# Kernel tuning notes

Hardware: AMD Instinct MI355X
Metric: run time of the kernel (lower is better)

## Reference

```python
import jax, jax.numpy as jnp
import numpy as np

H = 16          # num heads
HD = 64         # head dim
TEMPERATURE = 1.0
LN_EPS = 1e-5

def setup_inputs() -> dict:
    key = jax.random.key(0)
    ks = jax.random.split(key, 5)
    B, S, D = 2, 2048, 1024
    s = 1.0 / np.sqrt(D)
    return {
        "x": jax.random.normal(ks[0], (B, S, D), jnp.float32),
        "Wq": jax.random.normal(ks[1], (D, D), jnp.float32) * s,
        "bq": jnp.zeros((D,), jnp.float32),
        "Wk": jax.random.normal(ks[2], (D, D), jnp.float32) * s,
        "bk": jnp.zeros((D,), jnp.float32),
        "Wv": jax.random.normal(ks[3], (D, D), jnp.float32) * s,
        "bv": jnp.zeros((D,), jnp.float32),
        "Wo": jax.random.normal(ks[4], (D, D), jnp.float32) * s,
        "bo": jnp.zeros((D,), jnp.float32),
        "ln_gamma": jnp.ones((D,), jnp.float32),
        "ln_beta": jnp.zeros((D,), jnp.float32),
    }

def reference(x, Wq, bq, Wk, bk, Wv, bv, Wo, bo, ln_gamma, ln_beta):
    B, S, D = x.shape
    # LayerNorm (pre-attention)
    mu = jnp.mean(x, axis=-1, keepdims=True)
    var = jnp.mean(jnp.square(x - mu), axis=-1, keepdims=True)
    xn = (x - mu) * jax.lax.rsqrt(var + LN_EPS) * ln_gamma + ln_beta
    # Fused QKV projections (equivalent to H per-head Linears concatenated)
    q = (xn @ Wq + bq).reshape(B, S, H, HD)
    k = (xn @ Wk + bk).reshape(B, S, H, HD)
    v = (xn @ Wv + bv).reshape(B, S, H, HD)
    scale = np.sqrt(HD) * TEMPERATURE
    scores = jnp.einsum("bqhd,bkhd->bhqk", q, k) / scale
    attn = jax.nn.softmax(scores, axis=-1)  # dropout p=0 -> identity
    ctx = jnp.einsum("bhqk,bkhd->bqhd", attn, v).reshape(B, S, D)
    out = ctx @ Wo + bo
    return x + out
```

## Files before the change

### kernel.cpp

```cpp
#include <hip/hip_runtime.h>
#include <hip/hip_bf16.h>

#define Bc   2
#define Sc   2048
#define Dc   1024
#define Hc   16
#define HDc  64
#define MR   (Bc * Sc)
#define TBK  32

typedef __attribute__((ext_vector_type(8))) short bf16x8;
typedef __attribute__((ext_vector_type(4))) float f32x4;

__device__ __forceinline__ unsigned short f2bf(float f) {
    __hip_bfloat16 h = __float2bfloat16(f);
    return *reinterpret_cast<unsigned short*>(&h);
}

__device__ __forceinline__ void gll16(const unsigned short* g, unsigned short* l) {
    __builtin_amdgcn_global_load_lds(
        (__attribute__((address_space(1))) const unsigned int*)g,
        (__attribute__((address_space(3))) unsigned int*)l,
        16, 0, 0);
}

__global__ __launch_bounds__(256) void ln_kernel(const float* __restrict__ x,
                                                 const float* __restrict__ gamma,
                                                 const float* __restrict__ beta,
                                                 unsigned short* __restrict__ xn) {
    int row = blockIdx.x;
    int t = threadIdx.x;
    const float4* xr = (const float4*)(x + (size_t)row * Dc);
    float4 v = xr[t];
    float s  = v.x + v.y + v.z + v.w;
    float ss = v.x * v.x + v.y * v.y + v.z * v.z + v.w * v.w;
    #pragma unroll
    for (int off = 32; off; off >>= 1) {
        s  += __shfl_xor(s, off, 64);
        ss += __shfl_xor(ss, off, 64);
    }
    __shared__ float red[8];
    int w = t >> 6, lane = t & 63;
    if (lane == 0) { red[w * 2] = s; red[w * 2 + 1] = ss; }
    __syncthreads();
    s  = red[0] + red[2] + red[4] + red[6];
    ss = red[1] + red[3] + red[5] + red[7];
    float mean = s * (1.0f / Dc);
    float var  = ss * (1.0f / Dc) - mean * mean;
    float rstd = rsqrtf(var + 1e-5f);
    const float4* g4 = (const float4*)gamma;
    const float4* b4 = (const float4*)beta;
    float4 g = g4[t], bb = b4[t];
    ushort4 o;
    o.x = f2bf((v.x - mean) * rstd * g.x + bb.x);
    o.y = f2bf((v.y - mean) * rstd * g.y + bb.y);
    o.z = f2bf((v.z - mean) * rstd * g.z + bb.z);
    o.w = f2bf((v.w - mean) * rstd * g.w + bb.w);
    *(ushort4*)(xn + (size_t)row * Dc + t * 4) = o;
}

__global__ __launch_bounds__(256) void wcast_kernel(
        const float* __restrict__ W0, const float* __restrict__ W1,
        const float* __restrict__ W2, const float* __restrict__ W3,
        unsigned short* __restrict__ T0, unsigned short* __restrict__ T1,
        unsigned short* __restrict__ T2, unsigned short* __restrict__ T3) {
    int z = blockIdx.z;
    const float* W = (z == 0) ? W0 : (z == 1) ? W1 : (z == 2) ? W2 : W3;
    unsigned short* T = (z == 0) ? T0 : (z == 1) ? T1 : (z == 2) ? T2 : T3;
    __shared__ float tile[64][65];
    int kb = blockIdx.y * 64, nb = blockIdx.x * 64;
    int t = threadIdx.x;
    int r0 = t >> 4, c4 = (t & 15) * 4;
    #pragma unroll
    for (int rr = 0; rr < 4; rr++) {
        int row = rr * 16 + r0;
        float4 v = *(const float4*)(W + (size_t)(kb + row) * Dc + nb + c4);
        tile[row][c4 + 0] = v.x; tile[row][c4 + 1] = v.y;
        tile[row][c4 + 2] = v.z; tile[row][c4 + 3] = v.w;
    }
    __syncthreads();
    #pragma unroll
    for (int rr = 0; rr < 4; rr++) {
        int nrow = rr * 16 + r0;
        ushort4 o;
        o.x = f2bf(tile[c4 + 0][nrow]); o.y = f2bf(tile[c4 + 1][nrow]);
        o.z = f2bf(tile[c4 + 2][nrow]); o.w = f2bf(tile[c4 + 3][nrow]);
        *(ushort4*)(T + (size_t)(nb + nrow) * Dc + kb + c4) = o;
    }
}

__device__ __forceinline__ void gemm_core(const unsigned short* __restrict__ A,
                                          const unsigned short* __restrict__ Wt,
                                          unsigned short* As, unsigned short* Bs,
                                          int m0, int n0, f32x4 acc[4][4]) {
    int t = threadIdx.x;
    int w = t >> 6, lane = t & 63;
    int l16 = lane & 15, quad = lane >> 4;
    int wm = (w >> 1) * 64, wn = (w & 1) * 64;

    int srow = lane >> 2;
    int scol = (lane & 3) * 8;
    const unsigned short* Ag = A  + (size_t)(m0 + w * 16 + srow) * Dc + scol;
    const unsigned short* Bg = Wt + (size_t)(n0 + w * 16 + srow) * Dc + scol;
    unsigned short* Asw = As + (w * 16) * TBK;
    unsigned short* Bsw = Bs + (w * 16) * TBK;

    for (int k0 = 0; k0 < Dc; k0 += TBK) {
        gll16(Ag + k0, Asw);
        gll16(Ag + k0 + (size_t)64 * Dc, Asw + 64 * TBK);
        gll16(Bg + k0, Bsw);
        gll16(Bg + k0 + (size_t)64 * Dc, Bsw + 64 * TBK);
        __syncthreads();
        bf16x8 af[4], bfr[4];
        #pragma unroll
        for (int i = 0; i < 4; i++) {
            af[i]  = *(const bf16x8*)(As + (wm + i * 16 + l16) * TBK + quad * 8);
            bfr[i] = *(const bf16x8*)(Bs + (wn + i * 16 + l16) * TBK + quad * 8);
        }
        #pragma unroll
        for (int i = 0; i < 4; i++)
            #pragma unroll
            for (int j = 0; j < 4; j++)
                acc[i][j] = __builtin_amdgcn_mfma_f32_16x16x32_bf16(af[i], bfr[j], acc[i][j], 0, 0, 0);
        __syncthreads();
    }
}

__global__ __launch_bounds__(256) void gemm_qkv_kernel(
        const unsigned short* __restrict__ A,
        const unsigned short* __restrict__ Wqt, const unsigned short* __restrict__ Wkt,
        const unsigned short* __restrict__ Wvt,
        const float* __restrict__ bq, const float* __restrict__ bk,
        const float* __restrict__ bv,
        unsigned short* __restrict__ Qb, unsigned short* __restrict__ Kb,
        unsigned short* __restrict__ Vtb) {
    __shared__ unsigned short As[128 * TBK];
    __shared__ unsigned short Bs[128 * TBK];
    int z = blockIdx.z;
    const unsigned short* Wt = (z == 0) ? Wqt : (z == 1) ? Wkt : Wvt;
    const float* bias = (z == 0) ? bq : (z == 1) ? bk : bv;
    unsigned short* Out = (z == 0) ? Qb : (z == 1) ? Kb : Vtb;
    float outscale = (z == 0) ? 0.125f : 1.0f;

    int n0 = blockIdx.x * 128, m0 = blockIdx.y * 128;
    f32x4 acc[4][4];
    #pragma unroll
    for (int i = 0; i < 4; i++)
        #pragma unroll
        for (int j = 0; j < 4; j++) acc[i][j] = (f32x4){0.f, 0.f, 0.f, 0.f};

    gemm_core(A, Wt, As, Bs, m0, n0, acc);

    int t = threadIdx.x;
    int w = t >> 6, lane = t & 63;
    int l16 = lane & 15, quad = lane >> 4;
    int wm = (w >> 1) * 64, wn = (w & 1) * 64;
    int b = m0 >> 11;
    #pragma unroll
    for (int j = 0; j < 4; j++) {
        int col = n0 + wn + j * 16 + l16;
        float bb = bias[col];
        int h = col >> 6, d = col & 63;
        #pragma unroll
        for (int i = 0; i < 4; i++) {
            #pragma unroll
            for (int r = 0; r < 4; r++) {
                int row = m0 + wm + i * 16 + quad * 4 + r;
                int s = row & (Sc - 1);
                unsigned short v = f2bf((acc[i][j][r] + bb) * outscale);
                if (z != 2)
                    Out[(((size_t)(b * Hc + h)) * Sc + s) * HDc + d] = v;
                else
                    Out[(((size_t)(b * Hc + h)) * HDc + d) * Sc + s] = v;
            }
        }
    }
}

__global__ __launch_bounds__(256) void gemm_o_kernel(
        const unsigned short* __restrict__ A,
        const unsigned short* __restrict__ Wot,
        const float* __restrict__ bo, const float* __restrict__ resid,
        float* __restrict__ Out) {
    __shared__ unsigned short As[128 * TBK];
    __shared__ unsigned short Bs[128 * TBK];
    int n0 = blockIdx.x * 128, m0 = blockIdx.y * 128;
    f32x4 acc[4][4];
    #pragma unroll
    for (int i = 0; i < 4; i++)
        #pragma unroll
        for (int j = 0; j < 4; j++) acc[i][j] = (f32x4){0.f, 0.f, 0.f, 0.f};

    gemm_core(A, Wot, As, Bs, m0, n0, acc);

    int t = threadIdx.x;
    int w = t >> 6, lane = t & 63;
    int l16 = lane & 15, quad = lane >> 4;
    int wm = (w >> 1) * 64, wn = (w & 1) * 64;
    #pragma unroll
    for (int j = 0; j < 4; j++) {
        int col = n0 + wn + j * 16 + l16;
        float bb = bo[col];
        #pragma unroll
        for (int i = 0; i < 4; i++) {
            #pragma unroll
            for (int r = 0; r < 4; r++) {
                int row = m0 + wm + i * 16 + quad * 4 + r;
                size_t off = (size_t)row * Dc + col;
                Out[off] = acc[i][j][r] + bb + resid[off];
            }
        }
    }
}

#define BQa 64
#define BKa 64
#define LDP 72

__global__ __launch_bounds__(256, 4) void attn_mfma_kernel(
        const unsigned short* __restrict__ Q,
        const unsigned short* __restrict__ K,
        const unsigned short* __restrict__ Vt,
        unsigned short* __restrict__ O) {
    __shared__ unsigned short Ks[BKa * LDP];
    __shared__ unsigned short Vs[HDc * LDP];
    __shared__ unsigned short Ps[4 * 16 * LDP];

    int t = threadIdx.x;
    int w = t >> 6, lane = t & 63;
    int quad = lane >> 4, l16 = lane & 15;
    int q0 = blockIdx.x * BQa;
    int bh = blockIdx.y;
    size_t qkbase = (size_t)bh * Sc * HDc;
    size_t vbase  = (size_t)bh * HDc * Sc;

    const unsigned short* qrow = Q + qkbase + (size_t)(q0 + w * 16 + l16) * HDc + quad * 8;
    bf16x8 qf0 = *(const bf16x8*)(qrow);
    bf16x8 qf1 = *(const bf16x8*)(qrow + 32);

    f32x4 Oacc[4];
    #pragma unroll
    for (int n = 0; n < 4; n++) Oacc[n] = (f32x4){0.f, 0.f, 0.f, 0.f};
    float lacc = 0.f;

    int srow = t >> 2, sseg = t & 3;
    const unsigned short* Kg = K + qkbase;
    const unsigned short* Vg = Vt + vbase;
    unsigned short* pw = Ps + w * 16 * LDP;

    for (int kt = 0; kt < Sc / BKa; kt++) {
        int k0 = kt * BKa;
        const unsigned short* kgp = Kg + (size_t)(k0 + srow) * HDc + sseg * 16;
        const unsigned short* vgp = Vg + (size_t)srow * Sc + k0 + sseg * 16;
        bf16x8 kv0 = *(const bf16x8*)(kgp);
        bf16x8 kv1 = *(const bf16x8*)(kgp + 8);
        bf16x8 vv0 = *(const bf16x8*)(vgp);
        bf16x8 vv1 = *(const bf16x8*)(vgp + 8);
        __syncthreads();
        *(bf16x8*)(Ks + srow * LDP + sseg * 16)     = kv0;
        *(bf16x8*)(Ks + srow * LDP + sseg * 16 + 8) = kv1;
        *(bf16x8*)(Vs + srow * LDP + sseg * 16)     = vv0;
        *(bf16x8*)(Vs + srow * LDP + sseg * 16 + 8) = vv1;
        __syncthreads();

        f32x4 st[4];
        #pragma unroll
        for (int m = 0; m < 4; m++) {
            const unsigned short* kb = Ks + (m * 16 + l16) * LDP + quad * 8;
            bf16x8 kf0 = *(const bf16x8*)(kb);
            bf16x8 kf1 = *(const bf16x8*)(kb + 32);
            f32x4 s = (f32x4){0.f, 0.f, 0.f, 0.f};
            s = __builtin_amdgcn_mfma_f32_16x16x32_bf16(kf0, qf0, s, 0, 0, 0);
            s = __builtin_amdgcn_mfma_f32_16x16x32_bf16(kf1, qf1, s, 0, 0, 0);
            st[m] = s;
        }

        #pragma unroll
        for (int m = 0; m < 4; m++) {
            float p0 = __expf(st[m][0]);
            float p1 = __expf(st[m][1]);
            float p2 = __expf(st[m][2]);
            float p3 = __expf(st[m][3]);
            lacc += (p0 + p1) + (p2 + p3);
            ushort4 pk;
            pk.x = f2bf(p0); pk.y = f2bf(p1); pk.z = f2bf(p2); pk.w = f2bf(p3);
            *(ushort4*)(pw + l16 * LDP + m * 16 + quad * 4) = pk;
        }

        #pragma unroll
        for (int kk = 0; kk < 2; kk++) {
            bf16x8 pf = *(const bf16x8*)(pw + l16 * LDP + kk * 32 + quad * 8);
            #pragma unroll
            for (int n = 0; n < 4; n++) {
                bf16x8 vf = *(const bf16x8*)(Vs + (n * 16 + l16) * LDP + kk * 32 + quad * 8);
                Oacc[n] = __builtin_amdgcn_mfma_f32_16x16x32_bf16(pf, vf, Oacc[n], 0, 0, 0);
            }
        }
    }

    lacc += __shfl_xor(lacc, 16, 64);
    lacc += __shfl_xor(lacc, 32, 64);
    int b = bh >> 4, h = bh & 15;
    #pragma unroll
    for (int i = 0; i < 4; i++) {
        float li = __shfl(lacc, quad * 4 + i, 64);
        float rl = 1.0f / li;
        int q = q0 + w * 16 + quad * 4 + i;
        #pragma unroll
        for (int n = 0; n < 4; n++) {
            O[((size_t)(b * Sc + q)) * Dc + h * HDc + n * 16 + l16] = f2bf(Oacc[n][i] * rl);
        }
    }
}

extern "C" void kernel_launch(void* const* d_in, const int* in_sizes, int n_in,
                              void* d_out, int out_size, void* d_ws, size_t ws_size,
                              hipStream_t stream) {
    const float* x     = (const float*)d_in[0];
    const float* Wq    = (const float*)d_in[1];
    const float* bq    = (const float*)d_in[2];
    const float* Wk    = (const float*)d_in[3];
    const float* bk    = (const float*)d_in[4];
    const float* Wv    = (const float*)d_in[5];
    const float* bv    = (const float*)d_in[6];
    const float* Wo    = (const float*)d_in[7];
    const float* bo    = (const float*)d_in[8];
    const float* gamma = (const float*)d_in[9];
    const float* beta  = (const float*)d_in[10];
    float* out = (float*)d_out;

    unsigned short* us = (unsigned short*)d_ws;
    const size_t NE = (size_t)MR * Dc;
    const size_t WE = (size_t)Dc * Dc;
    unsigned short* xn  = us;
    unsigned short* Qb  = us + NE;
    unsigned short* Kb  = us + 2 * NE;
    unsigned short* Vtb = us + 3 * NE;
    unsigned short* ctx = us + 4 * NE;
    unsigned short* Wqt = us + 5 * NE;
    unsigned short* Wkt = Wqt + WE;
    unsigned short* Wvt = Wkt + WE;
    unsigned short* Wot = Wvt + WE;

    dim3 tgrid(16, 16, 4);
    wcast_kernel<<<tgrid, 256, 0, stream>>>(Wq, Wk, Wv, Wo, Wqt, Wkt, Wvt, Wot);

    ln_kernel<<<MR, 256, 0, stream>>>(x, gamma, beta, xn);

    dim3 qkvgrid(Dc / 128, MR / 128, 3);
    gemm_qkv_kernel<<<qkvgrid, 256, 0, stream>>>(xn, Wqt, Wkt, Wvt, bq, bk, bv,
                                                 Qb, Kb, Vtb);

    dim3 agrid(Sc / BQa, Bc * Hc);
    attn_mfma_kernel<<<agrid, 256, 0, stream>>>(Qb, Kb, Vtb, ctx);

    dim3 ogrid(Dc / 128, MR / 128);
    gemm_o_kernel<<<ogrid, 256, 0, stream>>>(ctx, Wot, bo, x, out);
}
```

Before: 222.5 us.

## Split attention key range across waves with direct global K/V loads and reduction

Restructures the attention kernel so each of the four waves owns all 64 queries but a different 32-key slice of each 128-key step. K and V fragments are read straight from global memory instead of being staged in shared memory, which removes the per-tile __syncthreads barriers. Partial outputs and row sums are then reduced across waves through shared memory at the end. The log2(e) factor is folded into the Q scale so the kernel can call exp2 directly. In exchange it uses more registers (16 accumulators per wave, occupancy hint lowered to 3), relies on cache for K/V reuse, and adds an epilogue reduction.

```diff
diff --git a/kernel.cpp b/kernel.cpp
--- a/kernel.cpp
+++ b/kernel.cpp
@@ -8,6 +8,7 @@
 #define HDc  64
 #define MR   (Bc * Sc)
 #define TBK  32
+#define LOG2E 1.44269504088896f
 
 typedef __attribute__((ext_vector_type(8))) short bf16x8;
 typedef __attribute__((ext_vector_type(4))) float f32x4;
@@ -140,7 +141,7 @@
     const unsigned short* Wt = (z == 0) ? Wqt : (z == 1) ? Wkt : Wvt;
     const float* bias = (z == 0) ? bq : (z == 1) ? bk : bv;
     unsigned short* Out = (z == 0) ? Qb : (z == 1) ? Kb : Vtb;
-    float outscale = (z == 0) ? 0.125f : 1.0f;
+    float outscale = (z == 0) ? (0.125f * LOG2E) : 1.0f;
 
     int n0 = blockIdx.x * 128, m0 = blockIdx.y * 128;
     f32x4 acc[4][4];
@@ -213,104 +214,136 @@
     }
 }
 
-#define BQa 64
-#define BKa 64
-#define LDP 72
-
-__global__ __launch_bounds__(256, 4) void attn_mfma_kernel(
+#define PSLD 40
+
+__global__ __launch_bounds__(256, 3) void attn_mfma_kernel(
         const unsigned short* __restrict__ Q,
         const unsigned short* __restrict__ K,
         const unsigned short* __restrict__ Vt,
         unsigned short* __restrict__ O) {
-    __shared__ unsigned short Ks[BKa * LDP];
-    __shared__ unsigned short Vs[HDc * LDP];
-    __shared__ unsigned short Ps[4 * 16 * LDP];
+    __shared__ f32x4 smem[2144];
+    unsigned short* Ps = (unsigned short*)smem;
+    float* Osc  = (float*)smem;
+    float* lred = ((float*)smem) + 2 * 64 * 65;
 
     int t = threadIdx.x;
     int w = t >> 6, lane = t & 63;
     int quad = lane >> 4, l16 = lane & 15;
-    int q0 = blockIdx.x * BQa;
+    int q0 = blockIdx.x * 64;
     int bh = blockIdx.y;
-    size_t qkbase = (size_t)bh * Sc * HDc;
-    size_t vbase  = (size_t)bh * HDc * Sc;
-
-    const unsigned short* qrow = Q + qkbase + (size_t)(q0 + w * 16 + l16) * HDc + quad * 8;
-    bf16x8 qf0 = *(const bf16x8*)(qrow);
-    bf16x8 qf1 = *(const bf16x8*)(qrow + 32);
-
-    f32x4 Oacc[4];
-    #pragma unroll
-    for (int n = 0; n < 4; n++) Oacc[n] = (f32x4){0.f, 0.f, 0.f, 0.f};
-    float lacc = 0.f;
-
-    int srow = t >> 2, sseg = t & 3;
-    const unsigned short* Kg = K + qkbase;
-    const unsigned short* Vg = Vt + vbase;
-    unsigned short* pw = Ps + w * 16 * LDP;
-
-    for (int kt = 0; kt < Sc / BKa; kt++) {
-        int k0 = kt * BKa;
-        const unsigned short* kgp = Kg + (size_t)(k0 + srow) * HDc + sseg * 16;
-        const unsigned short* vgp = Vg + (size_t)srow * Sc + k0 + sseg * 16;
-        bf16x8 kv0 = *(const bf16x8*)(kgp);
-        bf16x8 kv1 = *(const bf16x8*)(kgp + 8);
-        bf16x8 vv0 = *(const bf16x8*)(vgp);
-        bf16x8 vv1 = *(const bf16x8*)(vgp + 8);
-        __syncthreads();
-        *(bf16x8*)(Ks + srow * LDP + sseg * 16)     = kv0;
-        *(bf16x8*)(Ks + srow * LDP + sseg * 16 + 8) = kv1;
-        *(bf16x8*)(Vs + srow * LDP + sseg * 16)     = vv0;
-        *(bf16x8*)(Vs + srow * LDP + sseg * 16 + 8) = vv1;
-        __syncthreads();
-
-        f32x4 st[4];
-        #pragma unroll
-        for (int m = 0; m < 4; m++) {
-            const unsigned short* kb = Ks + (m * 16 + l16) * LDP + quad * 8;
-            bf16x8 kf0 = *(const bf16x8*)(kb);
-            bf16x8 kf1 = *(const bf16x8*)(kb + 32);
-            f32x4 s = (f32x4){0.f, 0.f, 0.f, 0.f};
-            s = __builtin_amdgcn_mfma_f32_16x16x32_bf16(kf0, qf0, s, 0, 0, 0);
-            s = __builtin_amdgcn_mfma_f32_16x16x32_bf16(kf1, qf1, s, 0, 0, 0);
-            st[m] = s;
-        }
-
-        #pragma unroll
-        for (int m = 0; m < 4; m++) {
-            float p0 = __expf(st[m][0]);
-            float p1 = __expf(st[m][1]);
-            float p2 = __expf(st[m][2]);
-            float p3 = __expf(st[m][3]);
-            lacc += (p0 + p1) + (p2 + p3);
-            ushort4 pk;
-            pk.x = f2bf(p0); pk.y = f2bf(p1); pk.z = f2bf(p2); pk.w = f2bf(p3);
-            *(ushort4*)(pw + l16 * LDP + m * 16 + quad * 4) = pk;
-        }
-
-        #pragma unroll
-        for (int kk = 0; kk < 2; kk++) {
-            bf16x8 pf = *(const bf16x8*)(pw + l16 * LDP + kk * 32 + quad * 8);
-            #pragma unroll
-            for (int n = 0; n < 4; n++) {
-                bf16x8 vf = *(const bf16x8*)(Vs + (n * 16 + l16) * LDP + kk * 32 + quad * 8);
-                Oacc[n] = __builtin_amdgcn_mfma_f32_16x16x32_bf16(pf, vf, Oacc[n], 0, 0, 0);
+    const unsigned short* Qh = Q  + (size_t)bh * Sc * HDc;
+    const unsigned short* Kh = K  + (size_t)bh * Sc * HDc;
+    const unsigned short* Vh = Vt + (size_t)bh * HDc * Sc;
+
+    bf16x8 qf[4][2];
+    #pragma unroll
+    for (int j = 0; j < 4; j++) {
+        const unsigned short* qr = Qh + (size_t)(q0 + j * 16 + l16) * HDc + quad * 8;
+        qf[j][0] = *(const bf16x8*)(qr);
+        qf[j][1] = *(const bf16x8*)(qr + 32);
+    }
+
+    f32x4 Oacc[4][4];
+    #pragma unroll
+    for (int i = 0; i < 4; i++)
+        #pragma unroll
+        for (int n = 0; n < 4; n++) Oacc[i][n] = (f32x4){0.f, 0.f, 0.f, 0.f};
+    float lacc[4] = {0.f, 0.f, 0.f, 0.f};
+
+    unsigned short* Psw = Ps + w * 64 * PSLD;
+
+    for (int kt = 0; kt < Sc / 128; kt++) {
+        int k0 = kt * 128 + w * 32;
+
+        #pragma unroll
+        for (int m = 0; m < 2; m++) {
+            const unsigned short* ka = Kh + (size_t)(k0 + m * 16 + l16) * HDc + quad * 8;
+            bf16x8 kf0 = *(const bf16x8*)(ka);
+            bf16x8 kf1 = *(const bf16x8*)(ka + 32);
+            #pragma unroll
+            for (int j = 0; j < 4; j++) {
+                f32x4 s = (f32x4){0.f, 0.f, 0.f, 0.f};
+                s = __builtin_amdgcn_mfma_f32_16x16x32_bf16(kf0, qf[j][0], s, 0, 0, 0);
+                s = __builtin_amdgcn_mfma_f32_16x16x32_bf16(kf1, qf[j][1], s, 0, 0, 0);
+                float p0 = __builtin_amdgcn_exp2f(s[0]);
+                float p1 = __builtin_amdgcn_exp2f(s[1]);
+                float p2 = __builtin_amdgcn_exp2f(s[2]);
+                float p3 = __builtin_amdgcn_exp2f(s[3]);
+                lacc[j] += (p0 + p1) + (p2 + p3);
+                ushort4 pk;
+                pk.x = f2bf(p0); pk.y = f2bf(p1); pk.z = f2bf(p2); pk.w = f2bf(p3);
+                *(ushort4*)(Psw + (j * 16 + l16) * PSLD + m * 16 + quad * 4) = pk;
             }
         }
-    }
-
-    lacc += __shfl_xor(lacc, 16, 64);
-    lacc += __shfl_xor(lacc, 32, 64);
+
+        bf16x8 pf[4], vf[4];
+        #pragma unroll
+        for (int i = 0; i < 4; i++)
+            pf[i] = *(const bf16x8*)(Psw + (i * 16 + l16) * PSLD + quad * 8);
+        #pragma unroll
+        for (int n = 0; n < 4; n++)
+            vf[n] = *(const bf16x8*)(Vh + (size_t)(n * 16 + l16) * Sc + k0 + quad * 8);
+        #pragma unroll
+        for (int i = 0; i < 4; i++)
+            #pragma unroll
+            for (int n = 0; n < 4; n++)
+                Oacc[i][n] = __builtin_amdgcn_mfma_f32_16x16x32_bf16(pf[i], vf[n], Oacc[i][n], 0, 0, 0);
+    }
+
+    #pragma unroll
+    for (int j = 0; j < 4; j++) {
+        lacc[j] += __shfl_xor(lacc[j], 16, 64);
+        lacc[j] += __shfl_xor(lacc[j], 32, 64);
+    }
+
+    __syncthreads();
+    if (quad == 0) {
+        #pragma unroll
+        for (int j = 0; j < 4; j++) lred[w * 64 + j * 16 + l16] = lacc[j];
+    }
+    if (w >= 2) {
+        float* od = Osc + (size_t)(w - 2) * 64 * 65;
+        #pragma unroll
+        for (int i = 0; i < 4; i++)
+            #pragma unroll
+            for (int n = 0; n < 4; n++)
+                #pragma unroll
+                for (int r = 0; r < 4; r++)
+                    od[(i * 16 + quad * 4 + r) * 65 + n * 16 + l16] = Oacc[i][n][r];
+    }
+    __syncthreads();
+    if (w < 2) {
+        float* od = Osc + (size_t)w * 64 * 65;
+        #pragma unroll
+        for (int i = 0; i < 4; i++)
+            #pragma unroll
+            for (int n = 0; n < 4; n++)
+                #pragma unroll
+                for (int r = 0; r < 4; r++) {
+                    int idx = (i * 16 + quad * 4 + r) * 65 + n * 16 + l16;
+                    od[idx] = Oacc[i][n][r] + od[idx];
+                }
+    }
+    __syncthreads();
+
+    int q = t >> 2, d0 = (t & 3) * 16;
+    float l = lred[q] + lred[64 + q] + lred[128 + q] + lred[192 + q];
+    float rl = 1.0f / l;
+    bf16x8 o0, o1;
+    #pragma unroll
+    for (int dd = 0; dd < 8; dd++) {
+        float v = Osc[q * 65 + d0 + dd] + Osc[64 * 65 + q * 65 + d0 + dd];
+        o0[dd] = (short)f2bf(v * rl);
+    }
+    #pragma unroll
+    for (int dd = 0; dd < 8; dd++) {
+        float v = Osc[q * 65 + d0 + 8 + dd] + Osc[64 * 65 + q * 65 + d0 + 8 + dd];
+        o1[dd] = (short)f2bf(v * rl);
+    }
     int b = bh >> 4, h = bh & 15;
-    #pragma unroll
-    for (int i = 0; i < 4; i++) {
-        float li = __shfl(lacc, quad * 4 + i, 64);
-        float rl = 1.0f / li;
-        int q = q0 + w * 16 + quad * 4 + i;
-        #pragma unroll
-        for (int n = 0; n < 4; n++) {
-            O[((size_t)(b * Sc + q)) * Dc + h * HDc + n * 16 + l16] = f2bf(Oacc[n][i] * rl);
-        }
-    }
+    unsigned short* orow = O + (size_t)(b * Sc + q0 + q) * Dc + h * HDc + d0;
+    *(bf16x8*)(orow) = o0;
+    *(bf16x8*)(orow + 8) = o1;
 }
 
 extern "C" void kernel_launch(void* const* d_in, const int* in_sizes, int n_in,
@@ -351,7 +384,7 @@
     gemm_qkv_kernel<<<qkvgrid, 256, 0, stream>>>(xn, Wqt, Wkt, Wvt, bq, bk, bv,
                                                  Qb, Kb, Vtb);
 
-    dim3 agrid(Sc / BQa, Bc * Hc);
+    dim3 agrid(Sc / 64, Bc * Hc);
     attn_mfma_kernel<<<agrid, 256, 0, stream>>>(Qb, Kb, Vtb, ctx);
 
     dim3 ogrid(Dc / 128, MR / 128);
```

After: 243.0 us. +9.2%, slower.
